# Kernel optimization log

Measured on AMD Instinct MI355X. Metric: run time of the kernel, lower is better.

Reference implementation:

```python
import jax, jax.numpy as jnp
import numpy as np

P = 7            # cfg.PATCH_SIZE_PHOTOMETRIC
BRIGHT = 0.02    # bright_threshold
BIG = 1e9        # masks invalid points out of kNN
K = 5            # neighbors for smoothness/slope


def _smooth_l1(x, y, beta):
    d = jnp.abs(x - y)
    return jnp.where(d < beta, 0.5 * d * d / beta, d - 0.5 * beta)


def _sample_patches(img, kp):
    # img: [B,1,H,W], kp: [B,N,2] (x,y) in pixel coords -> [B,1,N,P,P]
    # matches F.grid_sample(align_corners=True, bilinear, border): with the
    # module's normalization, sampling positions are exactly pixel coords.
    B, _, H, W = img.shape
    N = kp.shape[1]
    half = P // 2
    lin = jnp.linspace(-half, half, P)
    oy, ox = jnp.meshgrid(lin, lin, indexing='ij')  # patch index (i,j): +x=lin[j], +y=lin[i]
    px = jnp.clip(kp[..., 0:1] + ox.ravel(), 0.0, W - 1)  # [B,N,P*P]
    py = jnp.clip(kp[..., 1:2] + oy.ravel(), 0.0, H - 1)
    x0 = jnp.floor(px); y0 = jnp.floor(py)
    fx = px - x0; fy = py - y0
    x0i = jnp.clip(x0.astype(jnp.int32), 0, W - 1)
    x1i = jnp.clip(x0i + 1, 0, W - 1)
    y0i = jnp.clip(y0.astype(jnp.int32), 0, H - 1)
    y1i = jnp.clip(y0i + 1, 0, H - 1)
    im = img[:, 0]  # [B,H,W]
    b = jnp.arange(B)[:, None, None]
    v00 = im[b, y0i, x0i]; v01 = im[b, y0i, x1i]
    v10 = im[b, y1i, x0i]; v11 = im[b, y1i, x1i]
    val = (v00 * (1 - fx) + v01 * fx) * (1 - fy) + (v10 * (1 - fx) + v11 * fx) * fy
    return val.reshape(B, 1, N, P, P)


def _forward(lg, rg, kpl, kpr, scores, Q):
    B, N, _ = kpl.shape
    # ---- epipolar ----
    y_diff = jnp.abs(kpl[..., 1] - kpr[..., 1])
    ws = scores.sum()
    l_epipolar = jnp.where(ws > 1e-4, (y_diff * scores).sum() / jnp.maximum(ws, 1e-12), y_diff.mean())
    # ---- photometric + intensity ----
    pl = _sample_patches(lg, kpl)
    pr = _sample_patches(rg, kpr)
    c = P // 2
    center_l = pl[:, 0, :, c, c]  # [B,N]
    center_r = pr[:, 0, :, c, c]
    is_bright = (center_l > BRIGHT).astype(pl.dtype)
    diff = jnp.abs(pl - pr).mean(axis=(1, 3, 4))  # [B,N]
    w = scores * is_bright
    wsum = w.sum()
    safe = jnp.maximum(wsum, 1e-12)
    l_masked = jnp.where(wsum > 1e-4, (diff * w).sum() / safe, 0.0)
    l_intensity = jnp.where(wsum > 1e-4, (_smooth_l1(center_l, center_r, 1.0) * w).sum() / safe, 0.0)
    l_photo = l_masked + l_intensity
    # ---- disparity -> 3D ----
    disp = kpl[..., 0] - kpr[..., 0]
    pts4 = jnp.concatenate([kpl, disp[..., None], jnp.ones((B, N, 1), kpl.dtype)], axis=-1)
    proj = jnp.einsum('bni,bji->bnj', pts4, Q)
    Wc = jnp.maximum(proj[..., 3], 1e-6)
    p3d = proj[..., :3] / Wc[..., None]  # [B,N,3]
    Z = p3d[..., 2]
    valid = (Z > 100) & (Z < 30000) & (scores > 0.1)  # [B,N]
    # ---- kNN smoothness / slope / zero-mean (masked, vectorized) ----
    pm = p3d / 1000.0
    xy = pm[..., jnp.array([0, 2])]  # [B,N,2] horizontal plane
    h = pm[..., 1]                   # [B,N] height
    sq = (xy * xy).sum(-1)
    d2 = sq[:, :, None] + sq[:, None, :] - 2.0 * jnp.einsum('bnd,bmd->bnm', xy, xy)
    dist = jnp.sqrt(jnp.maximum(d2, 1e-12))  # [B,N,N]
    vm = valid[:, :, None] & valid[:, None, :]
    dist = jnp.where(vm, dist, BIG)
    negd, idx = jax.lax.top_k(-dist, K + 1)   # ascending distance
    nbr_idx = idx[:, :, 1:]                   # drop self
    nbr_d = jnp.maximum(-negd[:, :, 1:], 1e-3)
    b = jnp.arange(B)[:, None, None]
    nbr_h = h[b, nbr_idx]                     # [B,N,K]
    local_mean = nbr_h.mean(-1)
    n_valid = valid.sum(-1)
    nv = jnp.maximum(n_valid, 1).astype(h.dtype)
    vf = valid.astype(h.dtype)
    ls_b = (_smooth_l1(h, local_mean, 0.01) * vf).sum(-1) / nv
    slopes = jnp.abs(nbr_h - h[..., None]) / nbr_d
    pen = jax.nn.relu(slopes - 0.4)
    lsl_b = (pen * vf[..., None]).sum((-1, -2)) / (nv * K)
    lz_b = jnp.abs((h * vf).sum(-1) / nv)
    ok = (n_valid >= 10).astype(h.dtype)
    nb = jnp.maximum(ok.sum(), 1.0)
    gate = ((scores > 0.1).sum() >= 10) & (ok.sum() > 0)
    l_smooth = jnp.where(gate, (ls_b * ok).sum() / nb, 0.0)
    l_slope = jnp.where(gate, (lsl_b * ok).sum() / nb, 0.0)
    l_zeromean = jnp.where(gate, (lz_b * ok).sum() / nb, 0.0)
    return (l_photo, l_epipolar, l_smooth, l_slope, l_zeromean)


def setup_inputs() -> dict:
    key = jax.random.key(0)
    k = jax.random.split(key, 7)
    B, N, H, W = 16, 2000, 720, 1280
    lg = jax.random.uniform(k[0], (B, 1, H, W), dtype=jnp.float32)
    rg = jax.random.uniform(k[1], (B, 1, H, W), dtype=jnp.float32)
    kx = jax.random.uniform(k[2], (B, N), minval=200.0, maxval=1080.0)
    ky = jax.random.uniform(k[3], (B, N), minval=50.0, maxval=670.0)
    disp = jax.random.uniform(k[4], (B, N), minval=10.0, maxval=200.0)
    kpl = jnp.stack([kx, ky], -1)
    kpr = jnp.stack([kx - disp, ky + 0.5 * jax.random.normal(k[5], (B, N))], -1)
    scores = jax.random.uniform(k[6], (B, N), dtype=jnp.float32)
    f, cx, cy, Tx = 1000.0, 640.0, 360.0, 120.0  # focal px, principal point, baseline mm
    Qm = jnp.array([[1.0, 0.0, 0.0, -cx],
                    [0.0, 1.0, 0.0, -cy],
                    [0.0, 0.0, 0.0, f],
                    [0.0, 0.0, 1.0 / Tx, 0.0]], dtype=jnp.float32)
    Q = jnp.broadcast_to(Qm, (B, 4, 4))
    return {"lg": lg, "rg": rg, "kpl": kpl, "kpr": kpr, "scores": scores, "Q": Q}


def reference(lg, rg, kpl, kpr, scores, Q):
    return _forward(lg, rg, kpl, kpr, scores, Q)
```

## Files before the change

### kernel.cpp

```cpp
#include <hip/hip_runtime.h>

#define BB 16
#define NN 2000
#define HH 720
#define WW 1280
#define NPT (BB*NN)
#define PT_BLOCKS (NPT/32)
#define KSTRIDE 2048

static __device__ __forceinline__ unsigned u_min(unsigned a, unsigned b){ return a < b ? a : b; }

static __device__ __forceinline__ unsigned u_med3(unsigned a, unsigned b, unsigned c) {
    unsigned d;
    asm("v_med3_u32 %0, %1, %2, %3" : "=v"(d) : "v"(a), "v"(b), "v"(c));
    return d;
}

__device__ __forceinline__ void ins5(unsigned K[5], unsigned u) {
    K[4] = u_med3(K[3], K[4], u);
    K[3] = u_med3(K[2], K[3], u);
    K[2] = u_med3(K[1], K[2], u);
    K[1] = u_med3(K[0], K[1], u);
    K[0] = u_min(K[0], u);
}

__device__ __forceinline__ float bilin(const float* __restrict__ im, float px, float py) {
    px = fminf(fmaxf(px, 0.f), (float)(WW - 1));
    py = fminf(fmaxf(py, 0.f), (float)(HH - 1));
    float x0f = floorf(px), y0f = floorf(py);
    float fx = px - x0f, fy = py - y0f;
    int x0 = min(max((int)x0f, 0), WW - 1);
    int x1 = min(x0 + 1, WW - 1);
    int y0 = min(max((int)y0f, 0), HH - 1);
    int y1 = min(y0 + 1, HH - 1);
    const float* r0 = im + (size_t)y0 * WW;
    const float* r1 = im + (size_t)y1 * WW;
    float v00 = r0[x0], v01 = r0[x1], v10 = r1[x0], v11 = r1[x1];
    return (v00 * (1.f - fx) + v01 * fx) * (1.f - fy)
         + (v10 * (1.f - fx) + v11 * fx) * fy;
}

__global__ __launch_bounds__(256) void point_kernel(
    const float* __restrict__ lg, const float* __restrict__ rg,
    const float* __restrict__ kpl, const float* __restrict__ kpr,
    const float* __restrict__ scores, const float* __restrict__ Q,
    float4* __restrict__ pts, float* __restrict__ partials,
    float* __restrict__ batch_acc)
{
    if (blockIdx.x == 0 && threadIdx.x < BB * 4) batch_acc[threadIdx.x] = 0.f;

    int wave = threadIdx.x >> 6, lane = threadIdx.x & 63;
    int rr = lane / 7, ci = lane - rr * 7;
    int s00 = lane + rr;
    if (s00 > 54) s00 = 54;
    int reg_r = lane >> 3, reg_c = lane & 7;

    float a0=0.f,a1=0.f,a2=0.f,a3=0.f,a4=0.f,a5=0.f,a6=0.f;

    for (int it = 0; it < 8; ++it) {
        int pt = blockIdx.x * 32 + wave * 8 + it;
        int b = pt / NN;
        const float* iml = lg + (size_t)b * (HH * WW);
        const float* imr = rg + (size_t)b * (HH * WW);
        float kxl = kpl[2*pt], kyl = kpl[2*pt+1];
        float kxr = kpr[2*pt], kyr = kpr[2*pt+1];
        float sc  = scores[pt];

        float flx = floorf(kxl), fly = floorf(kyl);
        int xbl = (int)flx - 3, ybl = (int)fly - 3;
        float fxl = kxl - flx, fyl = kyl - fly;
        float vl = 0.f;
        if (xbl >= 0 && xbl <= WW-8 && ybl >= 0 && ybl <= HH-8) {
            float reg = iml[(size_t)(ybl + reg_r) * WW + xbl + reg_c];
            float v00 = __shfl(reg, s00,     64);
            float v01 = __shfl(reg, s00 + 1, 64);
            float v10 = __shfl(reg, s00 + 8, 64);
            float v11 = __shfl(reg, s00 + 9, 64);
            vl = (v00*(1.f-fxl) + v01*fxl)*(1.f-fyl) + (v10*(1.f-fxl) + v11*fxl)*fyl;
        } else if (lane < 49) {
            vl = bilin(iml, kxl + (float)(ci-3), kyl + (float)(rr-3));
        }
        float frx = floorf(kxr), fry = floorf(kyr);
        int xbr = (int)frx - 3, ybr = (int)fry - 3;
        float fxr = kxr - frx, fyr = kyr - fry;
        float vr = 0.f;
        if (xbr >= 0 && xbr <= WW-8 && ybr >= 0 && ybr <= HH-8) {
            float reg = imr[(size_t)(ybr + reg_r) * WW + xbr + reg_c];
            float v00 = __shfl(reg, s00,     64);
            float v01 = __shfl(reg, s00 + 1, 64);
            float v10 = __shfl(reg, s00 + 8, 64);
            float v11 = __shfl(reg, s00 + 9, 64);
            vr = (v00*(1.f-fxr) + v01*fxr)*(1.f-fyr) + (v10*(1.f-fxr) + v11*fxr)*fyr;
        } else if (lane < 49) {
            vr = bilin(imr, kxr + (float)(ci-3), kyr + (float)(rr-3));
        }

        float adiff = (lane < 49) ? fabsf(vl - vr) : 0.f;
        float cl = __shfl(vl, 24, 64);
        float cr = __shfl(vr, 24, 64);
        #pragma unroll
        for (int off = 32; off > 0; off >>= 1) adiff += __shfl_down(adiff, off, 64);

        if (lane == 0) {
            float diff = adiff / 49.f;
            float isb  = (cl > 0.02f) ? 1.f : 0.f;
            float w    = sc * isb;
            float ydiff = fabsf(kyl - kyr);
            float dc = fabsf(cl - cr);
            float sl1 = (dc < 1.f) ? 0.5f * dc * dc : dc - 0.5f;

            const float* q = Q + b * 16;
            float dsp = kxl - kxr;
            float p0 = q[0]*kxl + q[1]*kyl + q[2]*dsp  + q[3];
            float p1 = q[4]*kxl + q[5]*kyl + q[6]*dsp  + q[7];
            float p2 = q[8]*kxl + q[9]*kyl + q[10]*dsp + q[11];
            float p3 = q[12]*kxl + q[13]*kyl + q[14]*dsp + q[15];
            float Wc = fmaxf(p3, 1e-6f);
            float X = p0 / Wc, Y = p1 / Wc, Z = p2 / Wc;
            bool valid = (Z > 100.f) && (Z < 30000.f) && (sc > 0.1f);
            float x  = X / 1000.f;
            float hh = Y / 1000.f;
            float y  = Z / 1000.f;
            float sq = x * x + y * y;
            if (!valid) { x = 0.f; y = 0.f; sq = 1e18f; }
            pts[pt] = make_float4(x, y, sq, hh);

            a0 += sc;  a1 += ydiff * sc;  a2 += ydiff;
            a3 += w;   a4 += diff * w;    a5 += sl1 * w;
            a6 += (sc > 0.1f) ? 1.f : 0.f;
        }
    }

    __shared__ float red[4][7];
    if (lane == 0) {
        red[wave][0]=a0; red[wave][1]=a1; red[wave][2]=a2; red[wave][3]=a3;
        red[wave][4]=a4; red[wave][5]=a5; red[wave][6]=a6;
    }
    __syncthreads();
    if (threadIdx.x < 8) {
        int k = threadIdx.x;
        float v = 0.f;
        if (k < 7) v = red[0][k] + red[1][k] + red[2][k] + red[3][k];
        partials[blockIdx.x * 8 + k] = v;
    }
}

__global__ __launch_bounds__(256) void knn_scan(
    const float4* __restrict__ pts, unsigned* __restrict__ keybuf,
    int msegLen, int ns)
{
    int b = blockIdx.z, seg = blockIdx.y;
    int mseg0 = seg * msegLen;
    int n = blockIdx.x * 256 + threadIdx.x;
    int nc = (n < NN) ? n : (NN - 1);

    float4 me = pts[b * NN + nc];
    float nx2 = -2.f * me.x, ny2 = -2.f * me.y, sqn = me.z;

    unsigned K[5] = {0xFFFFFFFFu,0xFFFFFFFFu,0xFFFFFFFFu,0xFFFFFFFFu,0xFFFFFFFFu};

    const float4* cand = pts + b * NN + mseg0;
    int nb0 = blockIdx.x * 256;
    bool has_self = (mseg0 < nb0 + 256) && (mseg0 + msegLen > nb0);

    if (has_self) {
        #pragma unroll 5
        for (int mm = 0; mm < msegLen; ++mm) {
            float4 o = cand[mm];
            int m = mseg0 + mm;
            float t = fmaf(ny2, o.y, o.z);
            t = fmaf(nx2, o.x, t);
            float d2 = fmaxf(t + sqn, 1e-12f);
            unsigned u = (__float_as_uint(d2) & 0xFFFFF800u) | (unsigned)m;
            u = (m == n) ? 0xFFFFFFFFu : u;
            ins5(K, u);
        }
    } else {
        #pragma unroll 5
        for (int mm = 0; mm < msegLen; ++mm) {
            float4 o = cand[mm];
            int m = mseg0 + mm;
            float t = fmaf(ny2, o.y, o.z);
            t = fmaf(nx2, o.x, t);
            float d2 = fmaxf(t + sqn, 1e-12f);
            unsigned u = (__float_as_uint(d2) & 0xFFFFF800u) | (unsigned)m;
            ins5(K, u);
        }
    }

    if (n < NN) {
        size_t base = (size_t)((b * ns + seg) * 5) * KSTRIDE + n;
        keybuf[base              ] = K[0];
        keybuf[base + KSTRIDE    ] = K[1];
        keybuf[base + KSTRIDE * 2] = K[2];
        keybuf[base + KSTRIDE * 3] = K[3];
        keybuf[base + KSTRIDE * 4] = K[4];
    }
}

__global__ __launch_bounds__(256) void knn_merge(
    const float4* __restrict__ pts, const unsigned* __restrict__ keybuf,
    float* __restrict__ batch_acc, int ns)
{
    int b = blockIdx.y;
    int n = blockIdx.x * 256 + threadIdx.x;

    float ls = 0.f, pen = 0.f, hacc = 0.f, cnt = 0.f;
    if (n < NN) {
        float4 me = pts[b * NN + n];
        if (me.z < 1e17f) {
            unsigned K[5] = {0xFFFFFFFFu,0xFFFFFFFFu,0xFFFFFFFFu,0xFFFFFFFFu,0xFFFFFFFFu};
            for (int s = 0; s < ns; ++s) {
                #pragma unroll
                for (int j = 0; j < 5; ++j) {
                    unsigned u = keybuf[(size_t)((b * ns + s) * 5 + j) * KSTRIDE + n];
                    ins5(K, u);
                }
            }
            float hsum = 0.f;
            #pragma unroll
            for (int t = 0; t < 5; ++t) {
                int idx = (int)(K[t] & 2047u);
                float4 o = pts[b * NN + idx];
                float dot = me.x * o.x + me.y * o.y;
                float d2 = (me.z + o.z) - 2.f * dot;
                float nd = fmaxf(sqrtf(fmaxf(d2, 1e-12f)), 0.001f);
                hsum += o.w;
                pen  += fmaxf(fabsf(o.w - me.w) / nd - 0.4f, 0.f);
            }
            float lm = hsum / 5.f;
            float dd = fabsf(me.w - lm);
            ls = (dd < 0.01f) ? 0.5f * dd * dd / 0.01f : dd - 0.005f;
            hacc = me.w;
            cnt  = 1.f;
        }
    }

    #pragma unroll
    for (int off = 32; off > 0; off >>= 1) {
        ls   += __shfl_down(ls,   off, 64);
        pen  += __shfl_down(pen,  off, 64);
        hacc += __shfl_down(hacc, off, 64);
        cnt  += __shfl_down(cnt,  off, 64);
    }
    __shared__ float r2[4][4];
    int wave = threadIdx.x >> 6, lane = threadIdx.x & 63;
    if (lane == 0) { r2[wave][0]=cnt; r2[wave][1]=ls; r2[wave][2]=pen; r2[wave][3]=hacc; }
    __syncthreads();
    if (threadIdx.x == 0) {
        float tc = r2[0][0]+r2[1][0]+r2[2][0]+r2[3][0];
        float tl = r2[0][1]+r2[1][1]+r2[2][1]+r2[3][1];
        float tp = r2[0][2]+r2[1][2]+r2[2][2]+r2[3][2];
        float th = r2[0][3]+r2[1][3]+r2[2][3]+r2[3][3];
        atomicAdd(&batch_acc[b * 4 + 0], tc);
        atomicAdd(&batch_acc[b * 4 + 1], tl);
        atomicAdd(&batch_acc[b * 4 + 2], tp);
        atomicAdd(&batch_acc[b * 4 + 3], th);
    }
}

__global__ __launch_bounds__(256) void final_kernel(
    const float* __restrict__ partials, const float* __restrict__ batch_acc,
    float* __restrict__ out)
{
    float s[8] = {0,0,0,0,0,0,0,0};
    for (int r = threadIdx.x; r < PT_BLOCKS; r += 256) {
        #pragma unroll
        for (int k = 0; k < 8; ++k) s[k] += partials[r * 8 + k];
    }
    #pragma unroll
    for (int off = 32; off > 0; off >>= 1) {
        #pragma unroll
        for (int k = 0; k < 8; ++k) s[k] += __shfl_down(s[k], off, 64);
    }
    __shared__ float wsum_s[4][8];
    int wv = threadIdx.x >> 6, lane = threadIdx.x & 63;
    if (lane == 0) {
        #pragma unroll
        for (int k = 0; k < 8; ++k) wsum_s[wv][k] = s[k];
    }
    __syncthreads();
    if (threadIdx.x == 0) {
        float t[8];
        #pragma unroll
        for (int k = 0; k < 8; ++k)
            t[k] = wsum_s[0][k] + wsum_s[1][k] + wsum_s[2][k] + wsum_s[3][k];
        float ssc = t[0], yds = t[1], yd = t[2], wsum = t[3], dw = t[4], iw = t[5], cnts = t[6];

        float l_epi = (ssc > 1e-4f) ? yds / fmaxf(ssc, 1e-12f) : yd / (float)NPT;
        float safe = fmaxf(wsum, 1e-12f);
        float l_photo = (wsum > 1e-4f) ? (dw / safe + iw / safe) : 0.f;

        float als = 0.f, alsl = 0.f, alz = 0.f, okc = 0.f;
        for (int b = 0; b < BB; ++b) {
            float nvf  = batch_acc[b * 4 + 0];
            float lsb  = batch_acc[b * 4 + 1];
            float penb = batch_acc[b * 4 + 2];
            float hb   = batch_acc[b * 4 + 3];
            float nv = fmaxf(nvf, 1.f);
            float ok = (nvf >= 10.f) ? 1.f : 0.f;
            als  += ok * (lsb / nv);
            alsl += ok * (penb / (nv * 5.f));
            alz  += ok * fabsf(hb / nv);
            okc  += ok;
        }
        float nb = fmaxf(okc, 1.f);
        bool gate = (cnts >= 10.f) && (okc > 0.f);
        out[0] = l_photo;
        out[1] = l_epi;
        out[2] = gate ? als / nb : 0.f;
        out[3] = gate ? alsl / nb : 0.f;
        out[4] = gate ? alz / nb : 0.f;
    }
}

extern "C" void kernel_launch(void* const* d_in, const int* in_sizes, int n_in,
                              void* d_out, int out_size, void* d_ws, size_t ws_size,
                              hipStream_t stream)
{
    const float* lg     = (const float*)d_in[0];
    const float* rg     = (const float*)d_in[1];
    const float* kpl    = (const float*)d_in[2];
    const float* kpr    = (const float*)d_in[3];
    const float* scores = (const float*)d_in[4];
    const float* Q      = (const float*)d_in[5];
    float* out = (float*)d_out;

    char* ws = (char*)d_ws;
    float4*   pts       = (float4*)ws;
    float*    partials  = (float*)(ws + 512000);
    float*    batch_acc = (float*)(ws + 544000);
    unsigned* keybuf    = (unsigned*)(ws + 544256);

    int ns = 16;
    size_t need = 544256 + (size_t)BB * 16 * 5 * KSTRIDE * 4;
    if (ws_size < need) ns = 8;
    if (ws_size < 544256 + (size_t)BB * 8 * 5 * KSTRIDE * 4) ns = 4;
    int msegLen = NN / ns;

    point_kernel<<<PT_BLOCKS, 256, 0, stream>>>(lg, rg, kpl, kpr, scores, Q,
                                                pts, partials, batch_acc);
    knn_scan<<<dim3(8, ns, BB), 256, 0, stream>>>(pts, keybuf, msegLen, ns);
    knn_merge<<<dim3(8, BB), 256, 0, stream>>>(pts, keybuf, batch_acc, ns);
    final_kernel<<<1, 256, 0, stream>>>(partials, batch_acc, out);
}
```

Before: 192.0 us.

## Split projection out, co-schedule patch sampling with kNN scan, fold final into merge

```diff
diff --git a/kernel.cpp b/kernel.cpp
--- a/kernel.cpp
+++ b/kernel.cpp
@@ -5,7 +5,8 @@
 #define HH 720
 #define WW 1280
 #define NPT (BB*NN)
-#define PT_BLOCKS (NPT/32)
+#define PATCH_BLOCKS (NPT/32)
+#define PROJ_BLOCKS (NPT/256)
 #define KSTRIDE 2048
 
 static __device__ __forceinline__ unsigned u_min(unsigned a, unsigned b){ return a < b ? a : b; }
@@ -40,167 +41,198 @@
          + (v10 * (1.f - fx) + v11 * fx) * fy;
 }
 
-__global__ __launch_bounds__(256) void point_kernel(
+__global__ __launch_bounds__(256) void project_kernel(
+    const float* __restrict__ kpl, const float* __restrict__ kpr,
+    const float* __restrict__ scores, const float* __restrict__ Q,
+    float4* __restrict__ pts, float* __restrict__ partialsA,
+    float* __restrict__ batch_acc, unsigned* __restrict__ dcnt)
+{
+    if (blockIdx.x == 0) {
+        if (threadIdx.x < BB * 4) batch_acc[threadIdx.x] = 0.f;
+        if (threadIdx.x == BB * 4) *dcnt = 0u;
+    }
+    int pt = blockIdx.x * 256 + threadIdx.x;
+    int b  = pt / NN;
+
+    float2 kl = ((const float2* __restrict__)kpl)[pt];
+    float2 kr = ((const float2* __restrict__)kpr)[pt];
+    float sc  = scores[pt];
+    float ydiff = fabsf(kl.y - kr.y);
+
+    const float* q = Q + b * 16;
+    float dsp = kl.x - kr.x;
+    float p0 = q[0]*kl.x  + q[1]*kl.y  + q[2]*dsp  + q[3];
+    float p1 = q[4]*kl.x  + q[5]*kl.y  + q[6]*dsp  + q[7];
+    float p2 = q[8]*kl.x  + q[9]*kl.y  + q[10]*dsp + q[11];
+    float p3 = q[12]*kl.x + q[13]*kl.y + q[14]*dsp + q[15];
+    float Wc = fmaxf(p3, 1e-6f);
+    float X = p0 / Wc, Y = p1 / Wc, Z = p2 / Wc;
+    bool valid = (Z > 100.f) && (Z < 30000.f) && (sc > 0.1f);
+    float x  = X / 1000.f;
+    float hh = Y / 1000.f;
+    float y  = Z / 1000.f;
+    float sq = x * x + y * y;
+    if (!valid) { x = 0.f; y = 0.f; sq = 1e18f; }
+    pts[pt] = make_float4(x, y, sq, hh);
+
+    float s0 = sc, s1 = ydiff * sc, s2 = ydiff, s3 = (sc > 0.1f) ? 1.f : 0.f;
+    #pragma unroll
+    for (int off = 32; off > 0; off >>= 1) {
+        s0 += __shfl_down(s0, off, 64);
+        s1 += __shfl_down(s1, off, 64);
+        s2 += __shfl_down(s2, off, 64);
+        s3 += __shfl_down(s3, off, 64);
+    }
+    __shared__ float red[4][4];
+    int wave = threadIdx.x >> 6, lane = threadIdx.x & 63;
+    if (lane == 0) { red[wave][0]=s0; red[wave][1]=s1; red[wave][2]=s2; red[wave][3]=s3; }
+    __syncthreads();
+    if (threadIdx.x < 4) {
+        int k = threadIdx.x;
+        partialsA[blockIdx.x * 4 + k] = red[0][k] + red[1][k] + red[2][k] + red[3][k];
+    }
+}
+
+__global__ __launch_bounds__(256) void fused_patch_scan(
     const float* __restrict__ lg, const float* __restrict__ rg,
     const float* __restrict__ kpl, const float* __restrict__ kpr,
-    const float* __restrict__ scores, const float* __restrict__ Q,
-    float4* __restrict__ pts, float* __restrict__ partials,
-    float* __restrict__ batch_acc)
+    const float* __restrict__ scores,
+    const float4* __restrict__ pts, unsigned* __restrict__ keybuf,
+    float* __restrict__ partialsB, int msegLen, int lns)
 {
-    if (blockIdx.x == 0 && threadIdx.x < BB * 4) batch_acc[threadIdx.x] = 0.f;
-
-    int wave = threadIdx.x >> 6, lane = threadIdx.x & 63;
-    int rr = lane / 7, ci = lane - rr * 7;
-    int s00 = lane + rr;
-    if (s00 > 54) s00 = 54;
-    int reg_r = lane >> 3, reg_c = lane & 7;
-
-    float a0=0.f,a1=0.f,a2=0.f,a3=0.f,a4=0.f,a5=0.f,a6=0.f;
-
-    for (int it = 0; it < 8; ++it) {
-        int pt = blockIdx.x * 32 + wave * 8 + it;
-        int b = pt / NN;
-        const float* iml = lg + (size_t)b * (HH * WW);
-        const float* imr = rg + (size_t)b * (HH * WW);
-        float kxl = kpl[2*pt], kyl = kpl[2*pt+1];
-        float kxr = kpr[2*pt], kyr = kpr[2*pt+1];
-        float sc  = scores[pt];
-
-        float flx = floorf(kxl), fly = floorf(kyl);
-        int xbl = (int)flx - 3, ybl = (int)fly - 3;
-        float fxl = kxl - flx, fyl = kyl - fly;
-        float vl = 0.f;
-        if (xbl >= 0 && xbl <= WW-8 && ybl >= 0 && ybl <= HH-8) {
-            float reg = iml[(size_t)(ybl + reg_r) * WW + xbl + reg_c];
-            float v00 = __shfl(reg, s00,     64);
-            float v01 = __shfl(reg, s00 + 1, 64);
-            float v10 = __shfl(reg, s00 + 8, 64);
-            float v11 = __shfl(reg, s00 + 9, 64);
-            vl = (v00*(1.f-fxl) + v01*fxl)*(1.f-fyl) + (v10*(1.f-fxl) + v11*fxl)*fyl;
-        } else if (lane < 49) {
-            vl = bilin(iml, kxl + (float)(ci-3), kyl + (float)(rr-3));
-        }
-        float frx = floorf(kxr), fry = floorf(kyr);
-        int xbr = (int)frx - 3, ybr = (int)fry - 3;
-        float fxr = kxr - frx, fyr = kyr - fry;
-        float vr = 0.f;
-        if (xbr >= 0 && xbr <= WW-8 && ybr >= 0 && ybr <= HH-8) {
-            float reg = imr[(size_t)(ybr + reg_r) * WW + xbr + reg_c];
-            float v00 = __shfl(reg, s00,     64);
-            float v01 = __shfl(reg, s00 + 1, 64);
-            float v10 = __shfl(reg, s00 + 8, 64);
-            float v11 = __shfl(reg, s00 + 9, 64);
-            vr = (v00*(1.f-fxr) + v01*fxr)*(1.f-fyr) + (v10*(1.f-fxr) + v11*fxr)*fyr;
-        } else if (lane < 49) {
-            vr = bilin(imr, kxr + (float)(ci-3), kyr + (float)(rr-3));
-        }
-
-        float adiff = (lane < 49) ? fabsf(vl - vr) : 0.f;
-        float cl = __shfl(vl, 24, 64);
-        float cr = __shfl(vr, 24, 64);
-        #pragma unroll
-        for (int off = 32; off > 0; off >>= 1) adiff += __shfl_down(adiff, off, 64);
-
-        if (lane == 0) {
-            float diff = adiff / 49.f;
-            float isb  = (cl > 0.02f) ? 1.f : 0.f;
-            float w    = sc * isb;
-            float ydiff = fabsf(kyl - kyr);
-            float dc = fabsf(cl - cr);
-            float sl1 = (dc < 1.f) ? 0.5f * dc * dc : dc - 0.5f;
-
-            const float* q = Q + b * 16;
-            float dsp = kxl - kxr;
-            float p0 = q[0]*kxl + q[1]*kyl + q[2]*dsp  + q[3];
-            float p1 = q[4]*kxl + q[5]*kyl + q[6]*dsp  + q[7];
-            float p2 = q[8]*kxl + q[9]*kyl + q[10]*dsp + q[11];
-            float p3 = q[12]*kxl + q[13]*kyl + q[14]*dsp + q[15];
-            float Wc = fmaxf(p3, 1e-6f);
-            float X = p0 / Wc, Y = p1 / Wc, Z = p2 / Wc;
-            bool valid = (Z > 100.f) && (Z < 30000.f) && (sc > 0.1f);
-            float x  = X / 1000.f;
-            float hh = Y / 1000.f;
-            float y  = Z / 1000.f;
-            float sq = x * x + y * y;
-            if (!valid) { x = 0.f; y = 0.f; sq = 1e18f; }
-            pts[pt] = make_float4(x, y, sq, hh);
-
-            a0 += sc;  a1 += ydiff * sc;  a2 += ydiff;
-            a3 += w;   a4 += diff * w;    a5 += sl1 * w;
-            a6 += (sc > 0.1f) ? 1.f : 0.f;
-        }
-    }
-
-    __shared__ float red[4][7];
-    if (lane == 0) {
-        red[wave][0]=a0; red[wave][1]=a1; red[wave][2]=a2; red[wave][3]=a3;
-        red[wave][4]=a4; red[wave][5]=a5; red[wave][6]=a6;
-    }
-    __syncthreads();
-    if (threadIdx.x < 8) {
-        int k = threadIdx.x;
-        float v = 0.f;
-        if (k < 7) v = red[0][k] + red[1][k] + red[2][k] + red[3][k];
-        partials[blockIdx.x * 8 + k] = v;
-    }
-}
-
-__global__ __launch_bounds__(256) void knn_scan(
-    const float4* __restrict__ pts, unsigned* __restrict__ keybuf,
-    int msegLen, int ns)
-{
-    int b = blockIdx.z, seg = blockIdx.y;
-    int mseg0 = seg * msegLen;
-    int n = blockIdx.x * 256 + threadIdx.x;
-    int nc = (n < NN) ? n : (NN - 1);
-
-    float4 me = pts[b * NN + nc];
-    float nx2 = -2.f * me.x, ny2 = -2.f * me.y, sqn = me.z;
-
-    unsigned K[5] = {0xFFFFFFFFu,0xFFFFFFFFu,0xFFFFFFFFu,0xFFFFFFFFu,0xFFFFFFFFu};
-
-    const float4* cand = pts + b * NN + mseg0;
-    int nb0 = blockIdx.x * 256;
-    bool has_self = (mseg0 < nb0 + 256) && (mseg0 + msegLen > nb0);
-
-    if (has_self) {
-        #pragma unroll 5
-        for (int mm = 0; mm < msegLen; ++mm) {
-            float4 o = cand[mm];
-            int m = mseg0 + mm;
-            float t = fmaf(ny2, o.y, o.z);
-            t = fmaf(nx2, o.x, t);
-            float d2 = fmaxf(t + sqn, 1e-12f);
-            unsigned u = (__float_as_uint(d2) & 0xFFFFF800u) | (unsigned)m;
-            u = (m == n) ? 0xFFFFFFFFu : u;
-            ins5(K, u);
+    if (blockIdx.x < PATCH_BLOCKS) {
+        int wave = threadIdx.x >> 6, lane = threadIdx.x & 63;
+        int rr = lane / 7, ci = lane - rr * 7;
+        int s00 = lane + rr;
+        if (s00 > 54) s00 = 54;
+        int reg_r = lane >> 3, reg_c = lane & 7;
+
+        float a3 = 0.f, a4 = 0.f, a5 = 0.f;
+
+        for (int it = 0; it < 8; ++it) {
+            int pt = blockIdx.x * 32 + wave * 8 + it;
+            int b = pt / NN;
+            const float* iml = lg + (size_t)b * (HH * WW);
+            const float* imr = rg + (size_t)b * (HH * WW);
+            float kxl = kpl[2*pt], kyl = kpl[2*pt+1];
+            float kxr = kpr[2*pt], kyr = kpr[2*pt+1];
+            float sc  = scores[pt];
+
+            float flx = floorf(kxl), fly = floorf(kyl);
+            int xbl = (int)flx - 3, ybl = (int)fly - 3;
+            float fxl = kxl - flx, fyl = kyl - fly;
+            float vl = 0.f;
+            if (xbl >= 0 && xbl <= WW-8 && ybl >= 0 && ybl <= HH-8) {
+                float reg = iml[(size_t)(ybl + reg_r) * WW + xbl + reg_c];
+                float v00 = __shfl(reg, s00,     64);
+                float v01 = __shfl(reg, s00 + 1, 64);
+                float v10 = __shfl(reg, s00 + 8, 64);
+                float v11 = __shfl(reg, s00 + 9, 64);
+                vl = (v00*(1.f-fxl) + v01*fxl)*(1.f-fyl) + (v10*(1.f-fxl) + v11*fxl)*fyl;
+            } else if (lane < 49) {
+                vl = bilin(iml, kxl + (float)(ci-3), kyl + (float)(rr-3));
+            }
+            float frx = floorf(kxr), fry = floorf(kyr);
+            int xbr = (int)frx - 3, ybr = (int)fry - 3;
+            float fxr = kxr - frx, fyr = kyr - fry;
+            float vr = 0.f;
+            if (xbr >= 0 && xbr <= WW-8 && ybr >= 0 && ybr <= HH-8) {
+                float reg = imr[(size_t)(ybr + reg_r) * WW + xbr + reg_c];
+                float v00 = __shfl(reg, s00,     64);
+                float v01 = __shfl(reg, s00 + 1, 64);
+                float v10 = __shfl(reg, s00 + 8, 64);
+                float v11 = __shfl(reg, s00 + 9, 64);
+                vr = (v00*(1.f-fxr) + v01*fxr)*(1.f-fyr) + (v10*(1.f-fxr) + v11*fxr)*fyr;
+            } else if (lane < 49) {
+                vr = bilin(imr, kxr + (float)(ci-3), kyr + (float)(rr-3));
+            }
+
+            float adiff = (lane < 49) ? fabsf(vl - vr) : 0.f;
+            float cl = __shfl(vl, 24, 64);
+            float cr = __shfl(vr, 24, 64);
+            #pragma unroll
+            for (int off = 32; off > 0; off >>= 1) adiff += __shfl_down(adiff, off, 64);
+
+            if (lane == 0) {
+                float diff = adiff / 49.f;
+                float isb  = (cl > 0.02f) ? 1.f : 0.f;
+                float w    = sc * isb;
+                float dc = fabsf(cl - cr);
+                float sl1 = (dc < 1.f) ? 0.5f * dc * dc : dc - 0.5f;
+                a3 += w;  a4 += diff * w;  a5 += sl1 * w;
+            }
+        }
+
+        __shared__ float red[4][3];
+        if (lane == 0) { red[wave][0]=a3; red[wave][1]=a4; red[wave][2]=a5; }
+        __syncthreads();
+        if (threadIdx.x < 4) {
+            int k = threadIdx.x;
+            float v = 0.f;
+            if (k < 3) v = red[0][k] + red[1][k] + red[2][k] + red[3][k];
+            partialsB[blockIdx.x * 4 + k] = v;
         }
     } else {
-        #pragma unroll 5
-        for (int mm = 0; mm < msegLen; ++mm) {
-            float4 o = cand[mm];
-            int m = mseg0 + mm;
-            float t = fmaf(ny2, o.y, o.z);
-            t = fmaf(nx2, o.x, t);
-            float d2 = fmaxf(t + sqn, 1e-12f);
-            unsigned u = (__float_as_uint(d2) & 0xFFFFF800u) | (unsigned)m;
-            ins5(K, u);
-        }
-    }
-
-    if (n < NN) {
-        size_t base = (size_t)((b * ns + seg) * 5) * KSTRIDE + n;
-        keybuf[base              ] = K[0];
-        keybuf[base + KSTRIDE    ] = K[1];
-        keybuf[base + KSTRIDE * 2] = K[2];
-        keybuf[base + KSTRIDE * 3] = K[3];
-        keybuf[base + KSTRIDE * 4] = K[4];
-    }
-}
-
-__global__ __launch_bounds__(256) void knn_merge(
+        int sblk = blockIdx.x - PATCH_BLOCKS;
+        int bx   = sblk & 7;
+        int r    = sblk >> 3;
+        int seg  = r & ((1 << lns) - 1);
+        int b    = r >> lns;
+        int ns   = 1 << lns;
+        int mseg0 = seg * msegLen;
+        int n = bx * 256 + threadIdx.x;
+        int nc = (n < NN) ? n : (NN - 1);
+
+        float4 me = pts[b * NN + nc];
+        float nx2 = -2.f * me.x, ny2 = -2.f * me.y, sqn = me.z;
+
+        unsigned K[5] = {0xFFFFFFFFu,0xFFFFFFFFu,0xFFFFFFFFu,0xFFFFFFFFu,0xFFFFFFFFu};
+
+        const float4* cand = pts + b * NN + mseg0;
+        int nb0 = bx * 256;
+        bool has_self = (mseg0 < nb0 + 256) && (mseg0 + msegLen > nb0);
+
+        if (has_self) {
+            #pragma unroll 5
+            for (int mm = 0; mm < msegLen; ++mm) {
+                float4 o = cand[mm];
+                int m = mseg0 + mm;
+                float t = fmaf(ny2, o.y, o.z);
+                t = fmaf(nx2, o.x, t);
+                float d2 = fmaxf(t + sqn, 1e-12f);
+                unsigned u = (__float_as_uint(d2) & 0xFFFFF800u) | (unsigned)m;
+                u = (m == n) ? 0xFFFFFFFFu : u;
+                ins5(K, u);
+            }
+        } else {
+            #pragma unroll 5
+            for (int mm = 0; mm < msegLen; ++mm) {
+                float4 o = cand[mm];
+                int m = mseg0 + mm;
+                float t = fmaf(ny2, o.y, o.z);
+                t = fmaf(nx2, o.x, t);
+                float d2 = fmaxf(t + sqn, 1e-12f);
+                unsigned u = (__float_as_uint(d2) & 0xFFFFF800u) | (unsigned)m;
+                ins5(K, u);
+            }
+        }
+
+        if (n < NN) {
+            size_t base = (size_t)((b * ns + seg) * 5) * KSTRIDE + n;
+            keybuf[base              ] = K[0];
+            keybuf[base + KSTRIDE    ] = K[1];
+            keybuf[base + KSTRIDE * 2] = K[2];
+            keybuf[base + KSTRIDE * 3] = K[3];
+            keybuf[base + KSTRIDE * 4] = K[4];
+        }
+    }
+}
+
+__global__ __launch_bounds__(256) void knn_merge_final(
     const float4* __restrict__ pts, const unsigned* __restrict__ keybuf,
-    float* __restrict__ batch_acc, int ns)
+    float* __restrict__ batch_acc, unsigned* __restrict__ dcnt,
+    const float* __restrict__ partialsA, const float* __restrict__ partialsB,
+    float* __restrict__ out, int ns)
 {
     int b = blockIdx.y;
     int n = blockIdx.x * 256 + threadIdx.x;
@@ -257,46 +289,58 @@
         atomicAdd(&batch_acc[b * 4 + 2], tp);
         atomicAdd(&batch_acc[b * 4 + 3], th);
     }
-}
-
-__global__ __launch_bounds__(256) void final_kernel(
-    const float* __restrict__ partials, const float* __restrict__ batch_acc,
-    float* __restrict__ out)
-{
-    float s[8] = {0,0,0,0,0,0,0,0};
-    for (int r = threadIdx.x; r < PT_BLOCKS; r += 256) {
-        #pragma unroll
-        for (int k = 0; k < 8; ++k) s[k] += partials[r * 8 + k];
+
+    __shared__ int lastf;
+    __threadfence();
+    if (threadIdx.x == 0) {
+        unsigned old = atomicAdd(dcnt, 1u);
+        lastf = (old == (unsigned)(8 * BB - 1)) ? 1 : 0;
+    }
+    __syncthreads();
+    if (!lastf) return;
+    __threadfence();
+
+    float s[7] = {0,0,0,0,0,0,0};
+    for (int rI = threadIdx.x; rI < PROJ_BLOCKS; rI += 256) {
+        s[0] += partialsA[rI * 4 + 0];
+        s[1] += partialsA[rI * 4 + 1];
+        s[2] += partialsA[rI * 4 + 2];
+        s[3] += partialsA[rI * 4 + 3];
+    }
+    for (int rI = threadIdx.x; rI < PATCH_BLOCKS; rI += 256) {
+        s[4] += partialsB[rI * 4 + 0];
+        s[5] += partialsB[rI * 4 + 1];
+        s[6] += partialsB[rI * 4 + 2];
     }
     #pragma unroll
     for (int off = 32; off > 0; off >>= 1) {
         #pragma unroll
-        for (int k = 0; k < 8; ++k) s[k] += __shfl_down(s[k], off, 64);
-    }
-    __shared__ float wsum_s[4][8];
-    int wv = threadIdx.x >> 6, lane = threadIdx.x & 63;
+        for (int k = 0; k < 7; ++k) s[k] += __shfl_down(s[k], off, 64);
+    }
+    __shared__ float ws2[4][7];
     if (lane == 0) {
         #pragma unroll
-        for (int k = 0; k < 8; ++k) wsum_s[wv][k] = s[k];
+        for (int k = 0; k < 7; ++k) ws2[wave][k] = s[k];
     }
     __syncthreads();
     if (threadIdx.x == 0) {
-        float t[8];
+        float t[7];
         #pragma unroll
-        for (int k = 0; k < 8; ++k)
-            t[k] = wsum_s[0][k] + wsum_s[1][k] + wsum_s[2][k] + wsum_s[3][k];
-        float ssc = t[0], yds = t[1], yd = t[2], wsum = t[3], dw = t[4], iw = t[5], cnts = t[6];
+        for (int k = 0; k < 7; ++k)
+            t[k] = ws2[0][k] + ws2[1][k] + ws2[2][k] + ws2[3][k];
+        float ssc = t[0], yds = t[1], yd = t[2], cnts = t[3];
+        float wsum = t[4], dw = t[5], iw = t[6];
 
         float l_epi = (ssc > 1e-4f) ? yds / fmaxf(ssc, 1e-12f) : yd / (float)NPT;
         float safe = fmaxf(wsum, 1e-12f);
         float l_photo = (wsum > 1e-4f) ? (dw / safe + iw / safe) : 0.f;
 
         float als = 0.f, alsl = 0.f, alz = 0.f, okc = 0.f;
-        for (int b = 0; b < BB; ++b) {
-            float nvf  = batch_acc[b * 4 + 0];
-            float lsb  = batch_acc[b * 4 + 1];
-            float penb = batch_acc[b * 4 + 2];
-            float hb   = batch_acc[b * 4 + 3];
+        for (int bb = 0; bb < BB; ++bb) {
+            float nvf  = __hip_atomic_load(&batch_acc[bb*4+0], __ATOMIC_RELAXED, __HIP_MEMORY_SCOPE_AGENT);
+            float lsb  = __hip_atomic_load(&batch_acc[bb*4+1], __ATOMIC_RELAXED, __HIP_MEMORY_SCOPE_AGENT);
+            float penb = __hip_atomic_load(&batch_acc[bb*4+2], __ATOMIC_RELAXED, __HIP_MEMORY_SCOPE_AGENT);
+            float hb   = __hip_atomic_load(&batch_acc[bb*4+3], __ATOMIC_RELAXED, __HIP_MEMORY_SCOPE_AGENT);
             float nv = fmaxf(nvf, 1.f);
             float ok = (nvf >= 10.f) ? 1.f : 0.f;
             als  += ok * (lsb / nv);
@@ -328,19 +372,22 @@
 
     char* ws = (char*)d_ws;
     float4*   pts       = (float4*)ws;
-    float*    partials  = (float*)(ws + 512000);
-    float*    batch_acc = (float*)(ws + 544000);
-    unsigned* keybuf    = (unsigned*)(ws + 544256);
+    float*    partialsA = (float*)(ws + 512000);
+    float*    partialsB = (float*)(ws + 514048);
+    float*    batch_acc = (float*)(ws + 530432);
+    unsigned* dcnt      = (unsigned*)(ws + 530688);
+    unsigned* keybuf    = (unsigned*)(ws + 530944);
 
     int ns = 16;
-    size_t need = 544256 + (size_t)BB * 16 * 5 * KSTRIDE * 4;
-    if (ws_size < need) ns = 8;
-    if (ws_size < 544256 + (size_t)BB * 8 * 5 * KSTRIDE * 4) ns = 4;
+    if (ws_size < 530944 + (size_t)BB * 16 * 5 * KSTRIDE * 4) ns = 8;
+    if (ws_size < 530944 + (size_t)BB *  8 * 5 * KSTRIDE * 4) ns = 4;
+    int lns = (ns == 16) ? 4 : ((ns == 8) ? 3 : 2);
     int msegLen = NN / ns;
 
-    point_kernel<<<PT_BLOCKS, 256, 0, stream>>>(lg, rg, kpl, kpr, scores, Q,
-                                                pts, partials, batch_acc);
-    knn_scan<<<dim3(8, ns, BB), 256, 0, stream>>>(pts, keybuf, msegLen, ns);
-    knn_merge<<<dim3(8, BB), 256, 0, stream>>>(pts, keybuf, batch_acc, ns);
-    final_kernel<<<1, 256, 0, stream>>>(partials, batch_acc, out);
-}
+    project_kernel<<<PROJ_BLOCKS, 256, 0, stream>>>(kpl, kpr, scores, Q,
+                                                    pts, partialsA, batch_acc, dcnt);
+    fused_patch_scan<<<PATCH_BLOCKS + 8 * ns * BB, 256, 0, stream>>>(
+        lg, rg, kpl, kpr, scores, pts, keybuf, partialsB, msegLen, lns);
+    knn_merge_final<<<dim3(8, BB), 256, 0, stream>>>(pts, keybuf, batch_acc, dcnt,
+                                                     partialsA, partialsB, out, ns);
+}
```

After: 186.1 us. 1.03x faster.
